# Performance work log

Hardware: AMD Instinct MI355X
Metric: run time of the kernel (lower is better)

The kernel has to match this reference:

```python
import jax, jax.numpy as jnp
import numpy as np
import math

DIM = 512
D_STATE = 16
D_CONV = 4
EXPAND = 2
D_INNER = EXPAND * DIM
DT_RANK = math.ceil(DIM / 16)  # 'auto'
B_SZ = 4
N_TOK = 4097


def setup_inputs() -> dict:
    key = jax.random.key(0)
    ks = jax.random.split(key, 12)
    s = 0.02
    x = jax.random.normal(ks[0], (B_SZ, N_TOK, DIM), dtype=jnp.float32)
    q_w = jax.random.normal(ks[1], (DIM, DIM), dtype=jnp.float32) * s
    in_proj_w = jax.random.normal(ks[2], (2 * D_INNER, DIM), dtype=jnp.float32) * s
    conv_w = jax.random.normal(ks[3], (D_INNER, D_CONV), dtype=jnp.float32) * s
    conv_b = jnp.zeros((D_INNER,), dtype=jnp.float32)
    x_proj_w = jax.random.normal(ks[4], (DT_RANK + 2 * D_STATE, D_INNER), dtype=jnp.float32) * s
    dt_w = jax.random.normal(ks[5], (D_INNER, DT_RANK), dtype=jnp.float32) * (DT_RANK ** -0.5)
    # dt bias: inverse softplus of dt sampled log-uniform in [dt_min, dt_max]
    dt = jnp.exp(jax.random.uniform(ks[6], (D_INNER,)) * (math.log(0.1) - math.log(0.001)) + math.log(0.001))
    dt_b = (dt + jnp.log(-jnp.expm1(-dt))).astype(jnp.float32)
    # A = 1..d_state per channel (S4D-real init)
    A_log = jnp.log(jnp.broadcast_to(jnp.arange(1, D_STATE + 1, dtype=jnp.float32), (D_INNER, D_STATE)))
    D = jnp.ones((D_INNER,), dtype=jnp.float32)
    out_proj_w = jax.random.normal(ks[7], (DIM, D_INNER), dtype=jnp.float32) * s
    proj_w = jax.random.normal(ks[8], (DIM, DIM), dtype=jnp.float32) * s
    proj_b = jnp.zeros((DIM,), dtype=jnp.float32)
    return {"x": x, "q_w": q_w, "in_proj_w": in_proj_w, "conv_w": conv_w, "conv_b": conv_b,
            "x_proj_w": x_proj_w, "dt_w": dt_w, "dt_b": dt_b, "A_log": A_log, "D": D,
            "out_proj_w": out_proj_w, "proj_w": proj_w, "proj_b": proj_b}


def _selective_scan(u, delta, A, Bm, Cm, D):
    # u, delta: (B, L, d); A: (d, n); Bm, Cm: (B, L, n); D: (d,)
    b, L, d = u.shape
    n = A.shape[1]

    def step(h, inp):
        u_t, d_t, b_t, c_t = inp  # (B,d) (B,d) (B,n) (B,n)
        dA = jnp.exp(d_t[..., None] * A)                      # (B, d, n)
        h = h * dA + (d_t * u_t)[..., None] * b_t[:, None, :]  # (B, d, n)
        y = jnp.einsum('bdn,bn->bd', h, c_t)
        return h, y

    h0 = jnp.zeros((b, d, n), dtype=u.dtype)
    _, ys = jax.lax.scan(step, h0, (u.transpose(1, 0, 2), delta.transpose(1, 0, 2),
                                    Bm.transpose(1, 0, 2), Cm.transpose(1, 0, 2)))
    return ys.transpose(1, 0, 2) + u * D  # (B, L, d)


def _mamba(tokens, in_proj_w, conv_w, conv_b, x_proj_w, dt_w, dt_b, A_log, D, out_proj_w):
    b, L, _ = tokens.shape
    xz = tokens @ in_proj_w.T                          # (B, L, 2*d_inner)
    xi, z = jnp.split(xz, 2, axis=-1)
    # causal depthwise conv1d over L
    xc = xi.transpose(0, 2, 1)                         # (B, d_inner, L)
    xc = jax.lax.conv_general_dilated(
        xc, conv_w[:, None, :], window_strides=(1,), padding=[(D_CONV - 1, 0)],
        feature_group_count=D_INNER)
    xc = xc + conv_b[None, :, None]
    xs = jax.nn.silu(xc.transpose(0, 2, 1))            # (B, L, d_inner)
    x_dbl = xs @ x_proj_w.T                            # (B, L, dt_rank + 2n)
    dt, Bm, Cm = jnp.split(x_dbl, [DT_RANK, DT_RANK + D_STATE], axis=-1)
    delta = jax.nn.softplus(dt @ dt_w.T + dt_b)        # (B, L, d_inner)
    A = -jnp.exp(A_log)                                # (d_inner, n)
    y = _selective_scan(xs, delta, A, Bm, Cm, D)
    y = y * jax.nn.silu(z)
    return y @ out_proj_w.T                            # (B, L, dim)


def reference(x, q_w, in_proj_w, conv_w, conv_b, x_proj_w, dt_w, dt_b, A_log, D, out_proj_w, proj_w, proj_b):
    cls_tok = x[:, :1, :]
    patch = x[:, 1:, :]
    q = cls_tok @ q_w.T
    tokens = jnp.concatenate([q, patch], axis=1)
    mixed = _mamba(tokens, in_proj_w, conv_w, conv_b, x_proj_w, dt_w, dt_b, A_log, D, out_proj_w)
    upd_cls = mixed[:, :1, :] @ proj_w.T + proj_b
    return jnp.concatenate([upd_cls, patch], axis=1)
```

## Files before the change

kernel.cpp:

```cpp
#include <hip/hip_runtime.h>
#include <math.h>


#define B_SZ 4
#define DIM 512
#define D_INNER 1024
#define L_TOK 4097
#define TOK_STRIDE (L_TOK * DIM)
#define PB4 (TOK_STRIDE / 4)
#define DT_RANK 32
#define D_STATE 16
#define CB 2040

#define SL0 0u
#define SL1 ((unsigned)PB4)
#define SL2 (2u * PB4)
#define SL3 (3u * PB4)
#define SL4 (4u * PB4)

__device__ __forceinline__ float silu_f(float v) { return v / (1.f + expf(-v)); }
__device__ __forceinline__ float f4dot(float4 a, float4 b) {
    return a.x * b.x + a.y * b.y + a.z * b.z + a.w * b.w;
}
__device__ __forceinline__ float red16(float v) {
    v += __shfl_xor(v, 1, 64); v += __shfl_xor(v, 2, 64);
    v += __shfl_xor(v, 4, 64); v += __shfl_xor(v, 8, 64);
    return v;
}
__device__ __forceinline__ float red32(float v) {
    v = red16(v); v += __shfl_xor(v, 16, 64); return v;
}
__device__ __forceinline__ float sel4(int c, float a0, float a1, float a2, float a3) {
    return (c == 0) ? a0 : (c == 1) ? a1 : (c == 2) ? a2 : a3;
}

__device__ __forceinline__ void do_copy(const float4* __restrict__ x4,
                                        float4* __restrict__ o4,
                                        int cb_idx, unsigned beg, unsigned end) {
    const unsigned stride = (unsigned)CB * 256u;
    for (unsigned i = beg + (unsigned)cb_idx * 256u + threadIdx.x; i < end; i += stride) {
        unsigned r = i;
        if (r >= 2u * PB4) r -= 2u * PB4;
        if (r >= (unsigned)PB4) r -= (unsigned)PB4;
        if (r >= 128u) o4[i] = x4[i];
    }
}

__global__ void __launch_bounds__(256)
k1_q(const float* __restrict__ x, const float* __restrict__ q_w,
     float* __restrict__ q_ws, float4* __restrict__ o4) {
    const int blk = blockIdx.x, tid = threadIdx.x;
    if (blk >= 8) { do_copy((const float4*)x, o4, blk - 8, SL0, SL1); return; }
    __shared__ float cls[4 * DIM];
    {
        float4* cl4 = (float4*)cls;
        const float4* xg = (const float4*)x;
#pragma unroll
        for (int t = 0; t < 2; ++t) {
            int f = tid + t * 256;
            cl4[f] = xg[(size_t)(f >> 7) * PB4 + (f & 127)];
        }
    }
    __syncthreads();
    const int w = tid >> 6, lane = tid & 63, c = lane & 15, g = lane >> 4;
#pragma unroll
    for (int p = 0; p < 4; ++p) {
        int r = blk * 64 + w * 16 + p * 4 + g;
        const float4* wr = (const float4*)(q_w + (size_t)r * DIM);
        float a0 = 0, a1 = 0, a2 = 0, a3 = 0;
#pragma unroll
        for (int j = 0; j < 8; ++j) {
            float4 wv = wr[c + 16 * j];
            a0 += f4dot(wv, ((const float4*)(cls))[c + 16 * j]);
            a1 += f4dot(wv, ((const float4*)(cls + DIM))[c + 16 * j]);
            a2 += f4dot(wv, ((const float4*)(cls + 2 * DIM))[c + 16 * j]);
            a3 += f4dot(wv, ((const float4*)(cls + 3 * DIM))[c + 16 * j]);
        }
        a0 = red16(a0); a1 = red16(a1); a2 = red16(a2); a3 = red16(a3);
        if (c < 4) q_ws[c * DIM + r] = sel4(c, a0, a1, a2, a3);
    }
}

__global__ void __launch_bounds__(256)
k2_xz(const float* __restrict__ q_ws, const float* __restrict__ in_proj_w,
      const float* __restrict__ conv_w, const float* __restrict__ conv_b,
      float* __restrict__ xs_ws, float* __restrict__ gz_ws,
      const float4* __restrict__ x4, float4* __restrict__ o4) {
    const int blk = blockIdx.x, tid = threadIdx.x;
    if (blk >= 32) { do_copy(x4, o4, blk - 32, SL1, SL2); return; }
    __shared__ float q_lds[4 * DIM];
    {
        float4* ql = (float4*)q_lds;
        const float4* qg = (const float4*)q_ws;
        ql[tid] = qg[tid]; ql[tid + 256] = qg[tid + 256];
    }
    __syncthreads();
    const int w = tid >> 6, lane = tid & 63, c = lane & 15, g = lane >> 4;
#pragma unroll
    for (int p = 0; p < 4; ++p) {
        int r = blk * 64 + w * 16 + p * 4 + g;
        const float4* wr = (const float4*)(in_proj_w + (size_t)r * DIM);
        float a0 = 0, a1 = 0, a2 = 0, a3 = 0;
#pragma unroll
        for (int j = 0; j < 8; ++j) {
            float4 wv = wr[c + 16 * j];
            a0 += f4dot(wv, ((const float4*)(q_lds))[c + 16 * j]);
            a1 += f4dot(wv, ((const float4*)(q_lds + DIM))[c + 16 * j]);
            a2 += f4dot(wv, ((const float4*)(q_lds + 2 * DIM))[c + 16 * j]);
            a3 += f4dot(wv, ((const float4*)(q_lds + 3 * DIM))[c + 16 * j]);
        }
        a0 = red16(a0); a1 = red16(a1); a2 = red16(a2); a3 = red16(a3);
        if (c < 4) {
            float v = sel4(c, a0, a1, a2, a3);
            if (r < D_INNER)
                xs_ws[c * D_INNER + r] = silu_f(v * conv_w[r * 4 + 3] + conv_b[r]);
            else
                gz_ws[c * D_INNER + (r - D_INNER)] = silu_f(v);
        }
    }
}

__global__ void __launch_bounds__(256)
k4_out(const float* __restrict__ xs_ws, const float* __restrict__ gz_ws,
       const float* __restrict__ x_proj_w, const float* __restrict__ dt_w,
       const float* __restrict__ dt_b, const float* __restrict__ Dp,
       const float* __restrict__ out_proj_w, float* __restrict__ o_ws,
       const float4* __restrict__ x4, float4* __restrict__ o4) {
    const int blk = blockIdx.x, tid = threadIdx.x;
    if (blk >= 16) { do_copy(x4, o4, blk - 16, SL2, SL3); return; }
    __shared__ float xs_lds[4 * D_INNER];
    __shared__ float xd_lds[4 * 64];
    __shared__ float y_lds[4 * D_INNER];
    {
        float4* xl = (float4*)xs_lds;
        const float4* xg = (const float4*)xs_ws;
#pragma unroll
        for (int t = 0; t < 4; ++t) xl[tid + t * 256] = xg[tid + t * 256];
    }
    __syncthreads();
    const int w = tid >> 6, lane = tid & 63, c2 = lane & 31, g2 = lane >> 5;

#pragma unroll
    for (int p = 0; p < 8; ++p) {
        int r = p * 8 + w * 2 + g2;
        const float4* wr = (const float4*)(x_proj_w + (size_t)r * D_INNER);
        float a0 = 0, a1 = 0, a2 = 0, a3 = 0;
#pragma unroll
        for (int j = 0; j < 8; ++j) {
            float4 wv = wr[c2 + 32 * j];
            a0 += f4dot(wv, ((const float4*)(xs_lds))[c2 + 32 * j]);
            a1 += f4dot(wv, ((const float4*)(xs_lds + D_INNER))[c2 + 32 * j]);
            a2 += f4dot(wv, ((const float4*)(xs_lds + 2 * D_INNER))[c2 + 32 * j]);
            a3 += f4dot(wv, ((const float4*)(xs_lds + 3 * D_INNER))[c2 + 32 * j]);
        }
        a0 = red32(a0); a1 = red32(a1); a2 = red32(a2); a3 = red32(a3);
        if (c2 < 4) xd_lds[c2 * 64 + r] = sel4(c2, a0, a1, a2, a3);
    }
    __syncthreads();

    float S[4];
#pragma unroll
    for (int b = 0; b < 4; ++b) {
        float s = 0.f;
#pragma unroll
        for (int n = 0; n < D_STATE; ++n)
            s += xd_lds[b * 64 + 32 + n] * xd_lds[b * 64 + 48 + n];
        S[b] = s;
    }
#pragma unroll
    for (int qq = 0; qq < 4; ++qq) {
        int d = tid + qq * 256;
        const float4* dw = (const float4*)(dt_w + (size_t)d * DT_RANK);
        float4 dwv[8];
#pragma unroll
        for (int j = 0; j < 8; ++j) dwv[j] = dw[j];
        float Dd = Dp[d], db = dt_b[d];
#pragma unroll
        for (int b = 0; b < 4; ++b) {
            const float4* xd4 = (const float4*)(xd_lds + b * 64);
            float dp = db;
#pragma unroll
            for (int j = 0; j < 8; ++j) dp += f4dot(dwv[j], xd4[j]);
            float delta = (dp > 20.f) ? dp : log1pf(expf(dp));
            y_lds[b * D_INNER + d] =
                xs_lds[b * D_INNER + d] * (delta * S[b] + Dd) * gz_ws[b * D_INNER + d];
        }
    }
    __syncthreads();

#pragma unroll
    for (int p = 0; p < 4; ++p) {
        int r = blk * 32 + w * 8 + p * 2 + g2;
        const float4* wr = (const float4*)(out_proj_w + (size_t)r * D_INNER);
        float a0 = 0, a1 = 0, a2 = 0, a3 = 0;
#pragma unroll
        for (int j = 0; j < 8; ++j) {
            float4 wv = wr[c2 + 32 * j];
            a0 += f4dot(wv, ((const float4*)(y_lds))[c2 + 32 * j]);
            a1 += f4dot(wv, ((const float4*)(y_lds + D_INNER))[c2 + 32 * j]);
            a2 += f4dot(wv, ((const float4*)(y_lds + 2 * D_INNER))[c2 + 32 * j]);
            a3 += f4dot(wv, ((const float4*)(y_lds + 3 * D_INNER))[c2 + 32 * j]);
        }
        a0 = red32(a0); a1 = red32(a1); a2 = red32(a2); a3 = red32(a3);
        if (c2 < 4) o_ws[c2 * DIM + r] = sel4(c2, a0, a1, a2, a3);
    }
}

__global__ void __launch_bounds__(256)
k5_upd(const float* __restrict__ o_ws, const float* __restrict__ proj_w,
       const float* __restrict__ proj_b, float* __restrict__ out,
       const float4* __restrict__ x4, float4* __restrict__ o4) {
    const int blk = blockIdx.x, tid = threadIdx.x;
    if (blk >= 8) { do_copy(x4, o4, blk - 8, SL3, SL4); return; }
    __shared__ float o_lds[4 * DIM];
    {
        float4* ol = (float4*)o_lds;
        const float4* og = (const float4*)o_ws;
        ol[tid] = og[tid]; ol[tid + 256] = og[tid + 256];
    }
    __syncthreads();
    const int w = tid >> 6, lane = tid & 63, c = lane & 15, g = lane >> 4;
#pragma unroll
    for (int p = 0; p < 4; ++p) {
        int r = blk * 64 + w * 16 + p * 4 + g;
        const float4* wr = (const float4*)(proj_w + (size_t)r * DIM);
        float a0 = 0, a1 = 0, a2 = 0, a3 = 0;
#pragma unroll
        for (int j = 0; j < 8; ++j) {
            float4 wv = wr[c + 16 * j];
            a0 += f4dot(wv, ((const float4*)(o_lds))[c + 16 * j]);
            a1 += f4dot(wv, ((const float4*)(o_lds + DIM))[c + 16 * j]);
            a2 += f4dot(wv, ((const float4*)(o_lds + 2 * DIM))[c + 16 * j]);
            a3 += f4dot(wv, ((const float4*)(o_lds + 3 * DIM))[c + 16 * j]);
        }
        a0 = red16(a0); a1 = red16(a1); a2 = red16(a2); a3 = red16(a3);
        if (c < 4) out[(size_t)c * TOK_STRIDE + r] = sel4(c, a0, a1, a2, a3) + proj_b[r];
    }
}

extern "C" void kernel_launch(void* const* d_in, const int* in_sizes, int n_in,
                              void* d_out, int out_size, void* d_ws, size_t ws_size,
                              hipStream_t stream) {
    const float* x          = (const float*)d_in[0];
    const float* q_w        = (const float*)d_in[1];
    const float* in_proj_w  = (const float*)d_in[2];
    const float* conv_w     = (const float*)d_in[3];
    const float* conv_b     = (const float*)d_in[4];
    const float* x_proj_w   = (const float*)d_in[5];
    const float* dt_w       = (const float*)d_in[6];
    const float* dt_b       = (const float*)d_in[7];
    const float* Dp         = (const float*)d_in[9];
    const float* out_proj_w = (const float*)d_in[10];
    const float* proj_w     = (const float*)d_in[11];
    const float* proj_b     = (const float*)d_in[12];
    float* out = (float*)d_out;
    float* ws  = (float*)d_ws;

    float* q_ws  = ws;
    float* xs_ws = ws + 2048;
    float* gz_ws = ws + 6144;
    float* o_ws  = ws + 10240;

    const float4* x4 = (const float4*)x;
    float4* o4 = (float4*)out;

    k1_q  <<<8 + CB,  256, 0, stream>>>(x, q_w, q_ws, o4);
    k2_xz <<<32 + CB, 256, 0, stream>>>(q_ws, in_proj_w, conv_w, conv_b,
                                        xs_ws, gz_ws, x4, o4);
    k4_out<<<16 + CB, 256, 0, stream>>>(xs_ws, gz_ws, x_proj_w, dt_w, dt_b, Dp,
                                        out_proj_w, o_ws, x4, o4);
    k5_upd<<<8 + CB,  256, 0, stream>>>(o_ws, proj_w, proj_b, out, x4, o4);
}
```

Measured before the change: 152.4 us.

## Fuse four launches into three with split-K partials and atomic final reduction

```diff
diff --git a/kernel.cpp b/kernel.cpp
--- a/kernel.cpp
+++ b/kernel.cpp
@@ -10,25 +10,31 @@
 #define PB4 (TOK_STRIDE / 4)
 #define DT_RANK 32
 #define D_STATE 16
-#define CB 2040
+#define NCH 32
+#define NB 2048
+#define NCP (NB - NCH)
+
+#define OFF_PRAW 0
+#define OFF_XS   262144
+#define OFF_GZ   266240
+#define OFF_PXD  270336
+#define OFF_ACC  274432
+#define OFF_TKT  276480
 
 #define SL0 0u
-#define SL1 ((unsigned)PB4)
-#define SL2 (2u * PB4)
-#define SL3 (3u * PB4)
-#define SL4 (4u * PB4)
+#define SL1 839066u
+#define SL2 1573248u
+#define SL3 2097664u
 
 __device__ __forceinline__ float silu_f(float v) { return v / (1.f + expf(-v)); }
 __device__ __forceinline__ float f4dot(float4 a, float4 b) {
     return a.x * b.x + a.y * b.y + a.z * b.z + a.w * b.w;
 }
-__device__ __forceinline__ float red16(float v) {
+__device__ __forceinline__ float red32(float v) {
     v += __shfl_xor(v, 1, 64); v += __shfl_xor(v, 2, 64);
     v += __shfl_xor(v, 4, 64); v += __shfl_xor(v, 8, 64);
+    v += __shfl_xor(v, 16, 64);
     return v;
-}
-__device__ __forceinline__ float red32(float v) {
-    v = red16(v); v += __shfl_xor(v, 16, 64); return v;
 }
 __device__ __forceinline__ float sel4(int c, float a0, float a1, float a2, float a3) {
     return (c == 0) ? a0 : (c == 1) ? a1 : (c == 2) ? a2 : a3;
@@ -37,7 +43,7 @@
 __device__ __forceinline__ void do_copy(const float4* __restrict__ x4,
                                         float4* __restrict__ o4,
                                         int cb_idx, unsigned beg, unsigned end) {
-    const unsigned stride = (unsigned)CB * 256u;
+    const unsigned stride = (unsigned)NCP * 256u;
     for (unsigned i = beg + (unsigned)cb_idx * 256u + threadIdx.x; i < end; i += stride) {
         unsigned r = i;
         if (r >= 2u * PB4) r -= 2u * PB4;
@@ -47,194 +53,186 @@
 }
 
 __global__ void __launch_bounds__(256)
-k1_q(const float* __restrict__ x, const float* __restrict__ q_w,
-     float* __restrict__ q_ws, float4* __restrict__ o4) {
+kA(const float* __restrict__ x, const float* __restrict__ q_w,
+   const float* __restrict__ in_proj_w, float* __restrict__ ws,
+   float4* __restrict__ o4) {
     const int blk = blockIdx.x, tid = threadIdx.x;
-    if (blk >= 8) { do_copy((const float4*)x, o4, blk - 8, SL0, SL1); return; }
-    __shared__ float cls[4 * DIM];
-    {
-        float4* cl4 = (float4*)cls;
-        const float4* xg = (const float4*)x;
-#pragma unroll
-        for (int t = 0; t < 2; ++t) {
-            int f = tid + t * 256;
-            cl4[f] = xg[(size_t)(f >> 7) * PB4 + (f & 127)];
-        }
-    }
-    __syncthreads();
-    const int w = tid >> 6, lane = tid & 63, c = lane & 15, g = lane >> 4;
-#pragma unroll
-    for (int p = 0; p < 4; ++p) {
-        int r = blk * 64 + w * 16 + p * 4 + g;
-        const float4* wr = (const float4*)(q_w + (size_t)r * DIM);
-        float a0 = 0, a1 = 0, a2 = 0, a3 = 0;
-#pragma unroll
-        for (int j = 0; j < 8; ++j) {
-            float4 wv = wr[c + 16 * j];
-            a0 += f4dot(wv, ((const float4*)(cls))[c + 16 * j]);
-            a1 += f4dot(wv, ((const float4*)(cls + DIM))[c + 16 * j]);
-            a2 += f4dot(wv, ((const float4*)(cls + 2 * DIM))[c + 16 * j]);
-            a3 += f4dot(wv, ((const float4*)(cls + 3 * DIM))[c + 16 * j]);
-        }
-        a0 = red16(a0); a1 = red16(a1); a2 = red16(a2); a3 = red16(a3);
-        if (c < 4) q_ws[c * DIM + r] = sel4(c, a0, a1, a2, a3);
+    if (blk >= NCH) { do_copy((const float4*)x, o4, blk - NCH, SL0, SL1); return; }
+    __shared__ __align__(16) float cls[4 * DIM];
+    __shared__ __align__(16) float qseg[4 * 16];
+    {
+        float4* c4 = (float4*)cls;
+        const float4* x4 = (const float4*)x;
+#pragma unroll
+        for (int it = 0; it < 2; ++it) {
+            int f = tid + it * 256;
+            c4[f] = x4[(size_t)(f >> 7) * PB4 + (f & 127)];
+        }
+    }
+    __syncthreads();
+    {
+        int row = tid >> 4, b = (tid >> 2) & 3, part = tid & 3;
+        const float4* w = (const float4*)(q_w + (size_t)(blk * 16 + row) * DIM) + part * 32;
+        const float4* c = (const float4*)(cls + b * DIM) + part * 32;
+        float v = 0.f;
+#pragma unroll
+        for (int m = 0; m < 32; ++m) v += f4dot(w[m], c[m]);
+        v += __shfl_xor(v, 1, 64);
+        v += __shfl_xor(v, 2, 64);
+        if (part == 0) qseg[b * 16 + row] = v;
+    }
+    __syncthreads();
+    float* praw = ws + OFF_PRAW + blk * 8192;
+#pragma unroll
+    for (int rr = 0; rr < 8; ++rr) {
+        int r = tid + 256 * rr;
+        const float4* w = (const float4*)(in_proj_w + (size_t)r * DIM + blk * 16);
+        float4 w0 = w[0], w1 = w[1], w2 = w[2], w3 = w[3];
+#pragma unroll
+        for (int b = 0; b < 4; ++b) {
+            const float4* q4 = (const float4*)(qseg + b * 16);
+            praw[r * 4 + b] = f4dot(w0, q4[0]) + f4dot(w1, q4[1]) +
+                              f4dot(w2, q4[2]) + f4dot(w3, q4[3]);
+        }
     }
 }
 
 __global__ void __launch_bounds__(256)
-k2_xz(const float* __restrict__ q_ws, const float* __restrict__ in_proj_w,
-      const float* __restrict__ conv_w, const float* __restrict__ conv_b,
-      float* __restrict__ xs_ws, float* __restrict__ gz_ws,
-      const float4* __restrict__ x4, float4* __restrict__ o4) {
+kB(const float* __restrict__ conv_w, const float* __restrict__ conv_b,
+   const float* __restrict__ x_proj_w, float* __restrict__ ws,
+   const float4* __restrict__ x4, float4* __restrict__ o4) {
     const int blk = blockIdx.x, tid = threadIdx.x;
-    if (blk >= 32) { do_copy(x4, o4, blk - 32, SL1, SL2); return; }
-    __shared__ float q_lds[4 * DIM];
-    {
-        float4* ql = (float4*)q_lds;
-        const float4* qg = (const float4*)q_ws;
-        ql[tid] = qg[tid]; ql[tid + 256] = qg[tid + 256];
-    }
-    __syncthreads();
-    const int w = tid >> 6, lane = tid & 63, c = lane & 15, g = lane >> 4;
-#pragma unroll
-    for (int p = 0; p < 4; ++p) {
-        int r = blk * 64 + w * 16 + p * 4 + g;
-        const float4* wr = (const float4*)(in_proj_w + (size_t)r * DIM);
-        float a0 = 0, a1 = 0, a2 = 0, a3 = 0;
-#pragma unroll
-        for (int j = 0; j < 8; ++j) {
-            float4 wv = wr[c + 16 * j];
-            a0 += f4dot(wv, ((const float4*)(q_lds))[c + 16 * j]);
-            a1 += f4dot(wv, ((const float4*)(q_lds + DIM))[c + 16 * j]);
-            a2 += f4dot(wv, ((const float4*)(q_lds + 2 * DIM))[c + 16 * j]);
-            a3 += f4dot(wv, ((const float4*)(q_lds + 3 * DIM))[c + 16 * j]);
-        }
-        a0 = red16(a0); a1 = red16(a1); a2 = red16(a2); a3 = red16(a3);
-        if (c < 4) {
-            float v = sel4(c, a0, a1, a2, a3);
-            if (r < D_INNER)
-                xs_ws[c * D_INNER + r] = silu_f(v * conv_w[r * 4 + 3] + conv_b[r]);
-            else
-                gz_ws[c * D_INNER + (r - D_INNER)] = silu_f(v);
-        }
+    if (blk >= NCH) { do_copy(x4, o4, blk - NCH, SL1, SL2); return; }
+    __shared__ __align__(16) float seg[4][64];
+    {
+        int rr = tid >> 2, b = tid & 3;
+        int g = blk * 64 + rr;
+        float acc = 0.f;
+        const float* p = ws + OFF_PRAW + g * 4 + b;
+#pragma unroll 8
+        for (int s = 0; s < 32; ++s) acc += p[s * 8192];
+        float v = (g < D_INNER) ? silu_f(acc * conv_w[g * 4 + 3] + conv_b[g])
+                                : silu_f(acc);
+        seg[b][rr] = v;
+        if (g < D_INNER) ws[OFF_XS + b * D_INNER + g] = v;
+        else             ws[OFF_GZ + b * D_INNER + (g - D_INNER)] = v;
+    }
+    if (blk == 31) {
+        for (int m = tid; m < 2048; m += 256) ws[OFF_ACC + m] = 0.f;
+        if (tid == 0) ((unsigned*)(ws + OFF_TKT))[0] = 0u;
+    }
+    __syncthreads();
+    if (blk < 16) {
+        int row = tid >> 2, b = tid & 3;
+        const float4* w = (const float4*)(x_proj_w + (size_t)row * D_INNER + blk * 64);
+        const float4* xv = (const float4*)(&seg[b][0]);
+        float v = 0.f;
+#pragma unroll
+        for (int m = 0; m < 16; ++m) v += f4dot(w[m], xv[m]);
+        ws[OFF_PXD + blk * 256 + row * 4 + b] = v;
     }
 }
 
 __global__ void __launch_bounds__(256)
-k4_out(const float* __restrict__ xs_ws, const float* __restrict__ gz_ws,
-       const float* __restrict__ x_proj_w, const float* __restrict__ dt_w,
-       const float* __restrict__ dt_b, const float* __restrict__ Dp,
-       const float* __restrict__ out_proj_w, float* __restrict__ o_ws,
-       const float4* __restrict__ x4, float4* __restrict__ o4) {
+kC(const float* __restrict__ dt_w, const float* __restrict__ dt_b,
+   const float* __restrict__ Dp, const float* __restrict__ out_proj_w,
+   const float* __restrict__ proj_w, const float* __restrict__ proj_b,
+   float* __restrict__ ws, float* __restrict__ out,
+   const float4* __restrict__ x4, float4* __restrict__ o4) {
     const int blk = blockIdx.x, tid = threadIdx.x;
-    if (blk >= 16) { do_copy(x4, o4, blk - 16, SL2, SL3); return; }
-    __shared__ float xs_lds[4 * D_INNER];
-    __shared__ float xd_lds[4 * 64];
-    __shared__ float y_lds[4 * D_INNER];
-    {
-        float4* xl = (float4*)xs_lds;
-        const float4* xg = (const float4*)xs_ws;
-#pragma unroll
-        for (int t = 0; t < 4; ++t) xl[tid + t * 256] = xg[tid + t * 256];
-    }
-    __syncthreads();
-    const int w = tid >> 6, lane = tid & 63, c2 = lane & 31, g2 = lane >> 5;
-
-#pragma unroll
-    for (int p = 0; p < 8; ++p) {
-        int r = p * 8 + w * 2 + g2;
-        const float4* wr = (const float4*)(x_proj_w + (size_t)r * D_INNER);
-        float a0 = 0, a1 = 0, a2 = 0, a3 = 0;
-#pragma unroll
-        for (int j = 0; j < 8; ++j) {
-            float4 wv = wr[c2 + 32 * j];
-            a0 += f4dot(wv, ((const float4*)(xs_lds))[c2 + 32 * j]);
-            a1 += f4dot(wv, ((const float4*)(xs_lds + D_INNER))[c2 + 32 * j]);
-            a2 += f4dot(wv, ((const float4*)(xs_lds + 2 * D_INNER))[c2 + 32 * j]);
-            a3 += f4dot(wv, ((const float4*)(xs_lds + 3 * D_INNER))[c2 + 32 * j]);
-        }
-        a0 = red32(a0); a1 = red32(a1); a2 = red32(a2); a3 = red32(a3);
-        if (c2 < 4) xd_lds[c2 * 64 + r] = sel4(c2, a0, a1, a2, a3);
-    }
-    __syncthreads();
-
+    if (blk >= NCH) { do_copy(x4, o4, blk - NCH, SL2, SL3); return; }
+    __shared__ __align__(16) float xd[4][64];
+    __shared__ __align__(16) float y[4][D_INNER];
+    __shared__ __align__(16) float oseg[4][16];
+    __shared__ unsigned lastflag;
+    {
+        int r = tid >> 2, b = tid & 3;
+        float acc = 0.f;
+        const float* p = ws + OFF_PXD + r * 4 + b;
+#pragma unroll
+        for (int s = 0; s < 16; ++s) acc += p[s * 256];
+        xd[b][r] = acc;
+    }
+    __syncthreads();
     float S[4];
 #pragma unroll
     for (int b = 0; b < 4; ++b) {
         float s = 0.f;
 #pragma unroll
-        for (int n = 0; n < D_STATE; ++n)
-            s += xd_lds[b * 64 + 32 + n] * xd_lds[b * 64 + 48 + n];
+        for (int n = 0; n < D_STATE; ++n) s += xd[b][32 + n] * xd[b][48 + n];
         S[b] = s;
     }
 #pragma unroll
     for (int qq = 0; qq < 4; ++qq) {
         int d = tid + qq * 256;
         const float4* dw = (const float4*)(dt_w + (size_t)d * DT_RANK);
-        float4 dwv[8];
-#pragma unroll
-        for (int j = 0; j < 8; ++j) dwv[j] = dw[j];
+        float4 dv[8];
+#pragma unroll
+        for (int j = 0; j < 8; ++j) dv[j] = dw[j];
         float Dd = Dp[d], db = dt_b[d];
 #pragma unroll
         for (int b = 0; b < 4; ++b) {
-            const float4* xd4 = (const float4*)(xd_lds + b * 64);
+            const float4* xd4 = (const float4*)(&xd[b][0]);
             float dp = db;
 #pragma unroll
-            for (int j = 0; j < 8; ++j) dp += f4dot(dwv[j], xd4[j]);
+            for (int j = 0; j < 8; ++j) dp += f4dot(dv[j], xd4[j]);
             float delta = (dp > 20.f) ? dp : log1pf(expf(dp));
-            y_lds[b * D_INNER + d] =
-                xs_lds[b * D_INNER + d] * (delta * S[b] + Dd) * gz_ws[b * D_INNER + d];
-        }
-    }
-    __syncthreads();
-
-#pragma unroll
-    for (int p = 0; p < 4; ++p) {
-        int r = blk * 32 + w * 8 + p * 2 + g2;
-        const float4* wr = (const float4*)(out_proj_w + (size_t)r * D_INNER);
-        float a0 = 0, a1 = 0, a2 = 0, a3 = 0;
-#pragma unroll
-        for (int j = 0; j < 8; ++j) {
-            float4 wv = wr[c2 + 32 * j];
-            a0 += f4dot(wv, ((const float4*)(y_lds))[c2 + 32 * j]);
-            a1 += f4dot(wv, ((const float4*)(y_lds + D_INNER))[c2 + 32 * j]);
-            a2 += f4dot(wv, ((const float4*)(y_lds + 2 * D_INNER))[c2 + 32 * j]);
-            a3 += f4dot(wv, ((const float4*)(y_lds + 3 * D_INNER))[c2 + 32 * j]);
-        }
-        a0 = red32(a0); a1 = red32(a1); a2 = red32(a2); a3 = red32(a3);
-        if (c2 < 4) o_ws[c2 * DIM + r] = sel4(c2, a0, a1, a2, a3);
-    }
-}
-
-__global__ void __launch_bounds__(256)
-k5_upd(const float* __restrict__ o_ws, const float* __restrict__ proj_w,
-       const float* __restrict__ proj_b, float* __restrict__ out,
-       const float4* __restrict__ x4, float4* __restrict__ o4) {
-    const int blk = blockIdx.x, tid = threadIdx.x;
-    if (blk >= 8) { do_copy(x4, o4, blk - 8, SL3, SL4); return; }
-    __shared__ float o_lds[4 * DIM];
-    {
-        float4* ol = (float4*)o_lds;
-        const float4* og = (const float4*)o_ws;
-        ol[tid] = og[tid]; ol[tid + 256] = og[tid + 256];
-    }
-    __syncthreads();
-    const int w = tid >> 6, lane = tid & 63, c = lane & 15, g = lane >> 4;
-#pragma unroll
-    for (int p = 0; p < 4; ++p) {
-        int r = blk * 64 + w * 16 + p * 4 + g;
-        const float4* wr = (const float4*)(proj_w + (size_t)r * DIM);
-        float a0 = 0, a1 = 0, a2 = 0, a3 = 0;
-#pragma unroll
-        for (int j = 0; j < 8; ++j) {
-            float4 wv = wr[c + 16 * j];
-            a0 += f4dot(wv, ((const float4*)(o_lds))[c + 16 * j]);
-            a1 += f4dot(wv, ((const float4*)(o_lds + DIM))[c + 16 * j]);
-            a2 += f4dot(wv, ((const float4*)(o_lds + 2 * DIM))[c + 16 * j]);
-            a3 += f4dot(wv, ((const float4*)(o_lds + 3 * DIM))[c + 16 * j]);
-        }
-        a0 = red16(a0); a1 = red16(a1); a2 = red16(a2); a3 = red16(a3);
-        if (c < 4) out[(size_t)c * TOK_STRIDE + r] = sel4(c, a0, a1, a2, a3) + proj_b[r];
+            y[b][d] = ws[OFF_XS + b * D_INNER + d] * (delta * S[b] + Dd)
+                    * ws[OFF_GZ + b * D_INNER + d];
+        }
+    }
+    __syncthreads();
+    {
+        int w = tid >> 6, lane = tid & 63, c2 = lane & 31, g2 = lane >> 5;
+#pragma unroll
+        for (int p = 0; p < 2; ++p) {
+            int rl = p * 8 + w * 2 + g2;
+            int r = blk * 16 + rl;
+            const float4* wr = (const float4*)(out_proj_w + (size_t)r * D_INNER);
+            float a0 = 0, a1 = 0, a2 = 0, a3 = 0;
+#pragma unroll
+            for (int j = 0; j < 8; ++j) {
+                float4 wv = wr[c2 + 32 * j];
+                a0 += f4dot(wv, ((const float4*)&y[0][0])[c2 + 32 * j]);
+                a1 += f4dot(wv, ((const float4*)&y[1][0])[c2 + 32 * j]);
+                a2 += f4dot(wv, ((const float4*)&y[2][0])[c2 + 32 * j]);
+                a3 += f4dot(wv, ((const float4*)&y[3][0])[c2 + 32 * j]);
+            }
+            a0 = red32(a0); a1 = red32(a1); a2 = red32(a2); a3 = red32(a3);
+            if (c2 < 4) oseg[c2][rl] = sel4(c2, a0, a1, a2, a3);
+        }
+    }
+    __syncthreads();
+    {
+#pragma unroll
+        for (int rr = 0; rr < 2; ++rr) {
+            int r = tid * 2 + rr;
+            const float4* w = (const float4*)(proj_w + (size_t)r * DIM + blk * 16);
+            float4 w0 = w[0], w1 = w[1], w2 = w[2], w3 = w[3];
+#pragma unroll
+            for (int b = 0; b < 4; ++b) {
+                const float4* ov = (const float4*)(&oseg[b][0]);
+                float v = f4dot(w0, ov[0]) + f4dot(w1, ov[1]) +
+                          f4dot(w2, ov[2]) + f4dot(w3, ov[3]);
+                atomicAdd(ws + OFF_ACC + b * DIM + r, v);
+            }
+        }
+    }
+    __threadfence();
+    __syncthreads();
+    if (tid == 0) {
+        unsigned old = atomicAdd((unsigned*)(ws + OFF_TKT), 1u);
+        lastflag = (old == NCH - 1) ? 1u : 0u;
+    }
+    __syncthreads();
+    if (lastflag) {
+        __threadfence();
+#pragma unroll
+        for (int m = 0; m < 8; ++m) {
+            int idx = tid + m * 256;
+            int b = idx >> 9, r = idx & 511;
+            out[(size_t)b * TOK_STRIDE + r] = ws[OFF_ACC + b * DIM + r] + proj_b[r];
+        }
     }
 }
 
@@ -256,18 +254,11 @@
     float* out = (float*)d_out;
     float* ws  = (float*)d_ws;
 
-    float* q_ws  = ws;
-    float* xs_ws = ws + 2048;
-    float* gz_ws = ws + 6144;
-    float* o_ws  = ws + 10240;
-
     const float4* x4 = (const float4*)x;
     float4* o4 = (float4*)out;
 
-    k1_q  <<<8 + CB,  256, 0, stream>>>(x, q_w, q_ws, o4);
-    k2_xz <<<32 + CB, 256, 0, stream>>>(q_ws, in_proj_w, conv_w, conv_b,
-                                        xs_ws, gz_ws, x4, o4);
-    k4_out<<<16 + CB, 256, 0, stream>>>(xs_ws, gz_ws, x_proj_w, dt_w, dt_b, Dp,
-                                        out_proj_w, o_ws, x4, o4);
-    k5_upd<<<8 + CB,  256, 0, stream>>>(o_ws, proj_w, proj_b, out, x4, o4);
-}
+    kA<<<NB, 256, 0, stream>>>(x, q_w, in_proj_w, ws, o4);
+    kB<<<NB, 256, 0, stream>>>(conv_w, conv_b, x_proj_w, ws, x4, o4);
+    kC<<<NB, 256, 0, stream>>>(dt_w, dt_b, Dp, out_proj_w, proj_w, proj_b,
+                               ws, out, x4, o4);
+}
```

After: 140.8 us. -7.6%, faster.
